# Optimization experiments

Hardware: AMD Instinct MI355X
Metric: run time of the kernel (lower is better)

The kernel has to match this reference:

```python
import jax, jax.numpy as jnp
import numpy as np
from jax import lax

B, DIM, H, W = 2, 128, 192, 192
GS = [16, 32, 32, 48]          # group ratios [1,2,2,3]/8 of DIM
HID = int(DIM * 2.66)          # 340, Restormer-style hidden width


def _pool_mat(n_in, n_out):
    # torch AdaptiveAvgPool as an explicit linear map [n_out, n_in]
    P = np.zeros((n_out, n_in), np.float32)
    for o in range(n_out):
        s = (o * n_in) // n_out
        e = ((o + 1) * n_in + n_out - 1) // n_out
        P[o, s:e] = 1.0 / (e - s)
    return jnp.asarray(P)


def _ln(t, w, b):
    # WithBias LayerNorm over the channel dim of NCHW (== LN over last dim of b(hw)c)
    mu = t.mean(1, keepdims=True)
    var = ((t - mu) ** 2).mean(1, keepdims=True)
    return (t - mu) / jnp.sqrt(var + 1e-5) * w[None, :, None, None] + b[None, :, None, None]


def _c1x1(t, w):
    return jnp.einsum('oc,bchw->bohw', w, t)


def _dw3(t, w):
    return lax.conv_general_dilated(t, w, (1, 1), 'SAME',
                                    dimension_numbers=('NCHW', 'OIHW', 'NCHW'),
                                    feature_group_count=t.shape[1])


def _c1d(t, w, b):
    return jnp.einsum('oc,bcl->bol', w, t) + b[None, :, None]


def _gelu(t):
    return jax.nn.gelu(t, approximate=False)


def _forward(x, qv_cache, ln1_w, ln1_b, ln2_w, ln2_b, temperature, w_qkv, w_qkv_dw, w_proj,
             intra_down_w, intra_down_b, intra_up_w, intra_up_b, intra_gate_w, intra_gate_b,
             inter0_cw_w, inter0_cw_b, inter0_g_w, inter0_g_b,
             inter1_cw_w, inter1_cw_b, inter1_g_w, inter1_g_b,
             inter2_cw_w, inter2_cw_b, inter2_g_w, inter2_g_b,
             inter3_cw_w, inter3_cw_b, inter3_g_w, inter3_g_b,
             ffn_in_w, ffn_dw_w, ffn_out_w):
    b, c, h, w_ = x.shape
    hw = h * w_
    inter_p = [(inter0_cw_w, inter0_cw_b, inter0_g_w, inter0_g_b),
               (inter1_cw_w, inter1_cw_b, inter1_g_w, inter1_g_b),
               (inter2_cw_w, inter2_cw_b, inter2_g_w, inter2_g_b),
               (inter3_cw_w, inter3_cw_b, inter3_g_w, inter3_g_b)]
    # ---- attention branch ----
    xn = _ln(x, ln1_w, ln1_b)
    qkv = _dw3(_c1x1(xn, w_qkv), w_qkv_dw)
    q, k, v = jnp.split(qkv, 3, axis=1)
    q = q.reshape(b, c, hw); k = k.reshape(b, c, hw); v = v.reshape(b, c, hw)
    # correlation-based channel re-grouping (torch.corrcoef on batch-mean of q)
    cf = q.mean(0)                                   # [C, HW]
    xm = cf - cf.mean(1, keepdims=True)
    cov = xm @ xm.T
    dsd = jnp.sqrt(jnp.diagonal(cov))
    corr = cov / (dsd[:, None] * dsd[None, :])
    idx = jnp.argsort(-corr.mean(1))                 # descending mean similarity
    q = q[:, idx]; k = k[:, idx]; v = v[:, idx]
    atts, tmpc, outs = [], [], []
    start = 0
    for i, g in enumerate(GS):
        qg = q[:, start:start + g]; kg = k[:, start:start + g]; vg = v[:, start:start + g]
        start += g
        qn = qg / jnp.maximum(jnp.linalg.norm(qg, axis=-1, keepdims=True), 1e-12)
        kn = kg / jnp.maximum(jnp.linalg.norm(kg, axis=-1, keepdims=True), 1e-12)
        att = jax.nn.softmax(jnp.einsum('bcl,bdl->bcd', qn, kn) * temperature[i, 0, 0], axis=-1)
        tmpc.append(lax.stop_gradient(qn) + lax.stop_gradient(kn))
        # Inter_CacheModulation: adaptive-pool cache to [g,g], FiLM + gated conv1d
        cw_w, cw_b, g_w, g_b = inter_p[i]
        P = _pool_mat(c, g)
        aligned = jnp.einsum('oi,bij,pj->bop', P, qv_cache, P)    # [1, g, g]
        scale, shift = jnp.split(_c1d(aligned + att, cw_w, cw_b), 2, axis=1)
        x1p = att * scale + shift
        att = x1p * _gelu(_c1d(x1p, g_w, g_b)) + att
        atts.append(att)
        outs.append(jnp.einsum('bcd,bdl->bcl', att, vg))
    # CalculateCurrentLayerCache: resize each group's batch-mean attn to [C,C].
    # Original does (u * c_i) // dim with c_i == dim, i.e. elementwise floor.
    acc = jnp.zeros((1, c, c), x.dtype)
    for a in atts:
        m = lax.stop_gradient(a).mean(0, keepdims=True)[:, None]  # [1,1,g,g]
        u = jax.image.resize(m, (1, 1, c, c), method='bilinear')
        acc = acc + jnp.floor(u)[:, 0]
    qv_new = qv_cache * 0.9 + acc * 0.1
    out_all = jnp.concatenate(outs, axis=1)          # [B, C, HW]
    tmp_all = jnp.concatenate(tmpc, axis=1)
    # Intra_CacheModulation
    s = tmp_all + out_all
    gated = _gelu(_c1d(s, intra_gate_w, intra_gate_b)) * s
    out_all = _c1d(_c1d(gated, intra_down_w, intra_down_b), intra_up_w, intra_up_b) + out_all
    x1 = x + _c1x1(out_all.reshape(b, c, h, w_), w_proj)
    # ---- gated-dconv FFN ----
    xn2 = _ln(x1, ln2_w, ln2_b)
    y1, y2 = jnp.split(_dw3(_c1x1(xn2, ffn_in_w), ffn_dw_w), 2, axis=1)
    out = x1 + _c1x1(_gelu(y1) * y2, ffn_out_w)
    return out, qv_new


def setup_inputs() -> dict:
    key = jax.random.key(0)
    ks = jax.random.split(key, 40)
    def w(i, shape, s=0.02):
        return jax.random.normal(ks[i], shape, jnp.float32) * s
    p = {}
    p['x'] = jax.random.normal(ks[0], (B, DIM, H, W), jnp.float32)
    p['qv_cache'] = jax.random.uniform(ks[1], (1, DIM, DIM), jnp.float32)
    p['ln1_w'] = jnp.ones((DIM,), jnp.float32); p['ln1_b'] = jnp.zeros((DIM,), jnp.float32)
    p['ln2_w'] = jnp.ones((DIM,), jnp.float32); p['ln2_b'] = jnp.zeros((DIM,), jnp.float32)
    p['temperature'] = jnp.ones((4, 1, 1), jnp.float32)
    p['w_qkv'] = w(2, (3 * DIM, DIM))
    p['w_qkv_dw'] = w(3, (3 * DIM, 1, 3, 3))
    p['w_proj'] = w(4, (DIM, DIM))
    p['intra_down_w'] = w(5, (DIM // 2, DIM)); p['intra_down_b'] = jnp.zeros((DIM // 2,), jnp.float32)
    p['intra_up_w'] = w(6, (DIM, DIM // 2)); p['intra_up_b'] = jnp.zeros((DIM,), jnp.float32)
    p['intra_gate_w'] = w(7, (DIM, DIM)); p['intra_gate_b'] = jnp.zeros((DIM,), jnp.float32)
    for i, g in enumerate(GS):
        p[f'inter{i}_cw_w'] = w(8 + 2 * i, (2 * g, g))
        p[f'inter{i}_cw_b'] = jnp.zeros((2 * g,), jnp.float32)
        p[f'inter{i}_g_w'] = w(9 + 2 * i, (g, g))
        p[f'inter{i}_g_b'] = jnp.zeros((g,), jnp.float32)
    p['ffn_in_w'] = w(20, (2 * HID, DIM))
    p['ffn_dw_w'] = w(21, (2 * HID, 1, 3, 3))
    p['ffn_out_w'] = w(22, (DIM, HID))
    return p


def reference(x, qv_cache, ln1_w, ln1_b, ln2_w, ln2_b, temperature, w_qkv, w_qkv_dw, w_proj,
              intra_down_w, intra_down_b, intra_up_w, intra_up_b, intra_gate_w, intra_gate_b,
              inter0_cw_w, inter0_cw_b, inter0_g_w, inter0_g_b,
              inter1_cw_w, inter1_cw_b, inter1_g_w, inter1_g_b,
              inter2_cw_w, inter2_cw_b, inter2_g_w, inter2_g_b,
              inter3_cw_w, inter3_cw_b, inter3_g_w, inter3_g_b,
              ffn_in_w, ffn_dw_w, ffn_out_w):
    return _forward(x, qv_cache, ln1_w, ln1_b, ln2_w, ln2_b, temperature, w_qkv, w_qkv_dw, w_proj,
                    intra_down_w, intra_down_b, intra_up_w, intra_up_b, intra_gate_w, intra_gate_b,
                    inter0_cw_w, inter0_cw_b, inter0_g_w, inter0_g_b,
                    inter1_cw_w, inter1_cw_b, inter1_g_w, inter1_g_b,
                    inter2_cw_w, inter2_cw_b, inter2_g_w, inter2_g_b,
                    inter3_cw_w, inter3_cw_b, inter3_g_w, inter3_g_b,
                    ffn_in_w, ffn_dw_w, ffn_out_w)
```

## Files before the change

### kernel.cpp

```cpp
#include <hip/hip_runtime.h>
#include <math.h>

#define TPB 256

constexpr int BN_  = 2;
constexpr int CDIM = 128;
constexpr int HH   = 192;
constexpr int WW   = 192;
constexpr int HWc  = HH * WW;
constexpr int C3   = 384;
constexpr int HID  = 340;
constexpr int NL2  = 288;
constexpr int CH2  = HWc / NL2;
constexpr int CV   = 288;

typedef unsigned short bf16_t;
typedef __attribute__((ext_vector_type(8))) __bf16 bf16x8;
typedef __attribute__((ext_vector_type(4))) float f32x4;

__device__ __forceinline__ float b2f(bf16_t v) {
  unsigned u = ((unsigned)v) << 16;
  return __uint_as_float(u);
}
__device__ __forceinline__ bf16_t f2b(float f) {
  unsigned u = __float_as_uint(f);
  unsigned r = (u + 0x7FFFu + ((u >> 16) & 1u)) >> 16;
  return (bf16_t)r;
}
__device__ __forceinline__ float ldf(const float* p) { return *p; }
__device__ __forceinline__ float ldf(const bf16_t* p) { return b2f(*p); }
__device__ __forceinline__ void stf(float* p, float v) { *p = v; }
__device__ __forceinline__ void stf(bf16_t* p, float v) { *p = f2b(v); }

__device__ __forceinline__ void ldv4(const float* p, float* v) {
  float4 t = *(const float4*)p;
  v[0] = t.x; v[1] = t.y; v[2] = t.z; v[3] = t.w;
}
__device__ __forceinline__ void ldv4(const bf16_t* p, float* v) {
  ushort4 t = *(const ushort4*)p;
  v[0] = b2f(t.x); v[1] = b2f(t.y); v[2] = b2f(t.z); v[3] = b2f(t.w);
}
__device__ __forceinline__ void stv4(float* p, const float* v) {
  float4 t; t.x = v[0]; t.y = v[1]; t.z = v[2]; t.w = v[3];
  *(float4*)p = t;
}
__device__ __forceinline__ void stv4(bf16_t* p, const float* v) {
  ushort4 t; t.x = f2b(v[0]); t.y = f2b(v[1]); t.z = f2b(v[2]); t.w = f2b(v[3]);
  *(ushort4*)p = t;
}

__device__ __forceinline__ float gelu_f(float x) {
  return 0.5f * x * (1.0f + erff(x * 0.7071067811865475f));
}

__device__ __forceinline__ void unpack8(uint4 v, float* rv) {
  unsigned wv[4] = {v.x, v.y, v.z, v.w};
#pragma unroll
  for (int j = 0; j < 8; ++j)
    rv[j + 1] = b2f((bf16_t)((wv[j >> 1] >> ((j & 1) * 16)) & 0xFFFFu));
}
__device__ __forceinline__ uint4 pack8(const float* a) {
  uint4 o;
  unsigned w[4];
#pragma unroll
  for (int p = 0; p < 4; ++p) {
    unsigned lo = f2b(a[2 * p]), hi = f2b(a[2 * p + 1]);
    w[p] = lo | (hi << 16);
  }
  o.x = w[0]; o.y = w[1]; o.z = w[2]; o.w = w[3];
  return o;
}
__device__ __forceinline__ float sum8(uint4 v) {
  unsigned w[4] = {v.x, v.y, v.z, v.w};
  float s = 0.f;
#pragma unroll
  for (int j = 0; j < 8; ++j)
    s += b2f((bf16_t)((w[j >> 1] >> ((j & 1) * 16)) & 0xFFFFu));
  return s;
}
__device__ __forceinline__ float sumsq8(uint4 v) {
  unsigned w[4] = {v.x, v.y, v.z, v.w};
  float s = 0.f;
#pragma unroll
  for (int j = 0; j < 8; ++j) {
    float t = b2f((bf16_t)((w[j >> 1] >> ((j & 1) * 16)) & 0xFFFFu));
    s += t * t;
  }
  return s;
}

__device__ __forceinline__ void dwrow(const bf16_t* rp, int w8, float* rv) {
  unpack8(*(const uint4*)rp, rv);
  rv[0] = (w8 > 0) ? b2f(rp[-1]) : 0.f;
  rv[9] = (w8 + 8 < WW) ? b2f(rp[8]) : 0.f;
}

__device__ __constant__ int dGSZ[4]   = {16, 32, 32, 48};
__device__ __constant__ int dGST[4]   = {0, 16, 48, 80};
__device__ __constant__ int dAOFF[4]  = {0, 256, 1280, 2304};
__device__ __constant__ int dABASE[4] = {0, 512, 2560, 4608};

constexpr size_t oATTRAW  = 0;
constexpr size_t oATTS2   = 65536;
constexpr size_t oMUP     = 102400;
constexpr size_t oWB      = 131072;
constexpr size_t oATTS    = 1327104;
constexpr size_t oNORMQ   = 1363968;
constexpr size_t oNORMK   = 1364992;
constexpr size_t oIDX     = 1366016;
constexpr size_t oMU      = 1366528;
constexpr size_t oCOV     = 1367040;
constexpr size_t oQKV     = 1572864;
constexpr size_t oXN      = 58195968;
constexpr size_t oOUTALL  = 77070336;
constexpr size_t oSBUF    = 95944704;
constexpr size_t WS_NEED  = 114819072;
constexpr size_t oCHUNK1  = oOUTALL;
constexpr size_t oCOVPART = oOUTALL;
constexpr size_t oCOVP2   = oSBUF;
constexpr size_t oQKPART  = oXN;
constexpr size_t oGATED   = oQKV;
constexpr size_t oDBUF    = oQKV + 18874368;
constexpr size_t oY0C     = oOUTALL;
constexpr size_t oZ       = oQKV;
constexpr size_t oX1B     = oXN;

constexpr int eWQ   = 0;
constexpr int eGATE = 49152;
constexpr int eDOWN = 65536;
constexpr int eUP   = 73728;
constexpr int ePROJ = 81920;
constexpr int eFFI  = 98304;
constexpr int eFFO  = 185344;
constexpr int eTOT  = 234496;

__global__ __launch_bounds__(TPB) void k_wcvt(const float* __restrict__ wq,
                                              const float* __restrict__ gate,
                                              const float* __restrict__ down,
                                              const float* __restrict__ up,
                                              const float* __restrict__ proj,
                                              const float* __restrict__ ffi,
                                              const float* __restrict__ ffo,
                                              bf16_t* __restrict__ wb) {
  int t = blockIdx.x * TPB + threadIdx.x;
  if (t >= eTOT) return;
  int u = t;
  if (u < 49152) { wb[eWQ + u] = f2b(wq[u]); return; }
  u -= 49152;
  if (u < 16384) { wb[eGATE + u] = f2b(gate[u]); return; }
  u -= 16384;
  if (u < 8192)  { wb[eDOWN + u] = f2b(down[u]); return; }
  u -= 8192;
  if (u < 8192)  { wb[eUP + u] = f2b(up[u]); return; }
  u -= 8192;
  if (u < 16384) { wb[ePROJ + u] = f2b(proj[u]); return; }
  u -= 16384;
  if (u < 87040) { wb[eFFI + u] = f2b(ffi[u]); return; }
  u -= 87040;
  {
    int o = u / 384, k = u - o * 384;
    wb[eFFO + u] = (k < HID) ? f2b(ffo[o * HID + k]) : (bf16_t)0;
  }
}

template <typename TI>
__global__ __launch_bounds__(TPB) void k_ln(const TI* __restrict__ x,
                                            const float* __restrict__ w,
                                            const float* __restrict__ bias,
                                            bf16_t* __restrict__ out) {
  int t = blockIdx.x * TPB + threadIdx.x;
  if (t >= BN_ * HWc) return;
  int b = t / HWc, l = t - b * HWc;
  const TI* xb = x + (size_t)b * CDIM * HWc + l;
  float s = 0.f, s2 = 0.f;
#pragma unroll 4
  for (int c = 0; c < CDIM; ++c) { float v = ldf(&xb[(size_t)c * HWc]); s += v; s2 += v * v; }
  float mu  = s * (1.f / CDIM);
  float var = s2 * (1.f / CDIM) - mu * mu;
  float inv = 1.f / sqrtf(var + 1e-5f);
  bf16_t* ob = out + (size_t)b * CDIM * HWc + l;
#pragma unroll 4
  for (int c = 0; c < CDIM; ++c)
    stf(&ob[(size_t)c * HWc], (ldf(&xb[(size_t)c * HWc]) - mu) * inv * w[c] + bias[c]);
}

template <typename TO, typename TA, int KT, int EPI>
__global__ __launch_bounds__(TPB) void k_mgA(const bf16_t* __restrict__ W,
                                             const bf16_t* __restrict__ W2, int osplit,
                                             const float* __restrict__ bias,
                                             const bf16_t* __restrict__ in,
                                             const TA* __restrict__ aux,
                                             TO* __restrict__ out, int O,
                                             int ibr, int obr, int abr) {
  constexpr int L  = HWc;
  constexpr int PK = KT + 8;
  constexpr int KH = KT / 2;
  constexpr int SH = (KT == 128) ? 6 : 5;
  __shared__ bf16_t At[128 * PK];
  __shared__ bf16_t Wt[64 * PK];
  int b = blockIdx.y;
  const bf16_t* inb  = in  + (size_t)b * ibr * L;
  const TA*     auxb = aux ? aux + (size_t)b * abr * L : nullptr;
  TO*           outb = out + (size_t)b * obr * L;
  int l0 = blockIdx.x * 128;
  int tid = threadIdx.x, lane = tid & 63, wid = tid >> 6;
  int wm = wid >> 1, wn = wid & 1;
  int cl = lane & 15, rg = lane >> 4;

#pragma unroll
  for (int r = 0; r < (KH * 16) / TPB; ++r) {
    int u  = tid + r * TPB;
    int k2 = u & (KH - 1), lb = u >> SH;
    int ka = k2 * 2;
    uint4 rowA = *(const uint4*)(&inb[(size_t)ka * L + l0 + lb * 8]);
    uint4 rowB = *(const uint4*)(&inb[(size_t)(ka + 1) * L + l0 + lb * 8]);
    unsigned wa[4] = {rowA.x, rowA.y, rowA.z, rowA.w};
    unsigned wb[4] = {rowB.x, rowB.y, rowB.z, rowB.w};
#pragma unroll
    for (int j = 0; j < 8; ++j) {
      unsigned va = (wa[j >> 1] >> ((j & 1) * 16)) & 0xFFFFu;
      unsigned vb = (wb[j >> 1] >> ((j & 1) * 16)) & 0xFFFFu;
      *(unsigned*)(&At[(lb * 8 + j) * PK + ka]) = va | (vb << 16);
    }
  }

  int noc = (O + 63) >> 6;
  for (int oc = 0; oc < noc; ++oc) {
    int o0 = oc * 64;
#pragma unroll
    for (int r = 0; r < (64 * KT / 8) / TPB; ++r) {
      int e = tid + r * TPB;
      int o = e / (KT / 8), k8 = (e % (KT / 8)) * 8;
      int og = o0 + o;
      uint4 wv = {0u, 0u, 0u, 0u};
      if (og < O) {
        const bf16_t* wrow = (og < osplit) ? (W + (size_t)og * KT)
                                           : (W2 + (size_t)(og - osplit) * KT);
        wv = *(const uint4*)(&wrow[k8]);
      }
      *(uint4*)(&Wt[o * PK + k8]) = wv;
    }
    __syncthreads();
    f32x4 acc[2][4];
#pragma unroll
    for (int m = 0; m < 2; ++m)
#pragma unroll
      for (int n = 0; n < 4; ++n) acc[m][n] = (f32x4){0.f, 0.f, 0.f, 0.f};
#pragma unroll
    for (int kk = 0; kk < KT / 32; ++kk) {
      int kof = kk * 32 + rg * 8;
      bf16x8 a[2], bfr[4];
#pragma unroll
      for (int m = 0; m < 2; ++m)
        a[m] = *(const bf16x8*)(&Wt[(wm * 32 + m * 16 + cl) * PK + kof]);
#pragma unroll
      for (int n = 0; n < 4; ++n)
        bfr[n] = *(const bf16x8*)(&At[(wn * 64 + n * 16 + cl) * PK + kof]);
#pragma unroll
// ... 25 lines not shown
          for (int r = 0; r < 4; ++r) v[r] = gelu_f(v[r]) * a4[r];
        } else if (EPI == 3) {
          int lloc = wn * 64 + n * 16 + rg * 4;
#pragma unroll
          for (int r = 0; r < 4; ++r)
            v[r] = gelu_f(v[r]) * b2f(At[(lloc + r) * PK + og]);
        }
        stv4(&outb[off], v);
      }
    }
  }
}

template <typename TO, typename TA, int EPI>
__global__ __launch_bounds__(TPB) void k_mgB(const bf16_t* __restrict__ Wb,
                                             const float* __restrict__ bias,
                                             const bf16_t* __restrict__ in,
                                             const TA* __restrict__ aux,
                                             TO* __restrict__ out, int O, int K,
                                             int ibr, int obr, int abr) {
  constexpr int L = HWc;
  constexpr int PK = 72, BK = 64, WSTR = 384;
  __shared__ bf16_t At[128 * PK];
  __shared__ bf16_t Wt[128 * PK];
  int b = blockIdx.y;
  const bf16_t* inb  = in  + (size_t)b * ibr * L;
  const TA*     auxb = aux ? aux + (size_t)b * abr * L : nullptr;
  TO*           outb = out + (size_t)b * obr * L;
  int l0 = blockIdx.x * 128;
  int tid = threadIdx.x, lane = tid & 63, wid = tid >> 6;
  int wm = wid >> 1, wn = wid & 1;
  int cl = lane & 15, rg = lane >> 4;

  f32x4 acc[4][4];
#pragma unroll
  for (int m = 0; m < 4; ++m)
#pragma unroll
    for (int n = 0; n < 4; ++n) acc[m][n] = (f32x4){0.f, 0.f, 0.f, 0.f};

  for (int k0 = 0; k0 < K; k0 += BK) {
#pragma unroll
    for (int r = 0; r < 2; ++r) {
      int u = tid + r * TPB;
      int k2 = u & 31, lb = u >> 5;
      int ka = k0 + k2 * 2;
      uint4 rowA = {0u,0u,0u,0u}, rowB = {0u,0u,0u,0u};
      if (ka < K)     rowA = *(const uint4*)(&inb[(size_t)ka * L + l0 + lb * 8]);
      if (ka + 1 < K) rowB = *(const uint4*)(&inb[(size_t)(ka + 1) * L + l0 + lb * 8]);
      unsigned wa[4] = {rowA.x, rowA.y, rowA.z, rowA.w};
      unsigned wb[4] = {rowB.x, rowB.y, rowB.z, rowB.w};
#pragma unroll
      for (int j = 0; j < 8; ++j) {
        unsigned va = (wa[j >> 1] >> ((j & 1) * 16)) & 0xFFFFu;
        unsigned vb = (wb[j >> 1] >> ((j & 1) * 16)) & 0xFFFFu;
        *(unsigned*)(&At[(lb * 8 + j) * PK + k2 * 2]) = va | (vb << 16);
      }
    }
#pragma unroll
    for (int r = 0; r < 4; ++r) {
      int e = tid + r * TPB;
      int o = e >> 3, k8 = (e & 7) * 8;
      uint4 wv = *(const uint4*)(&Wb[(size_t)o * WSTR + k0 + k8]);
      *(uint4*)(&Wt[o * PK + k8]) = wv;
    }
    __syncthreads();
#pragma unroll
    for (int kk = 0; kk < 2; ++kk) {
      int kof = kk * 32 + rg * 8;
      bf16x8 a[4], bfr[4];
#pragma unroll
      for (int m = 0; m < 4; ++m)
        a[m] = *(const bf16x8*)(&Wt[(wm * 64 + m * 16 + cl) * PK + kof]);
#pragma unroll
      for (int n = 0; n < 4; ++n)
        bfr[n] = *(const bf16x8*)(&At[(wn * 64 + n * 16 + cl) * PK + kof]);
#pragma unroll
      for (int m = 0; m < 4; ++m)
#pragma unroll
        for (int n = 0; n < 4; ++n)
          acc[m][n] = __builtin_amdgcn_mfma_f32_16x16x32_bf16(bfr[n], a[m], acc[m][n], 0, 0, 0);
    }
    __syncthreads();
  }
#pragma unroll
  for (int m = 0; m < 4; ++m) {
    int og = wm * 64 + m * 16 + cl;
    if (og >= O) continue;
    float bv = bias ? bias[og] : 0.f;
#pragma unroll
    for (int n = 0; n < 4; ++n) {
      int lcol = l0 + wn * 64 + n * 16 + rg * 4;
      size_t off = (size_t)og * L + lcol;
      float v[4];
#pragma unroll
      for (int r = 0; r < 4; ++r) v[r] = acc[m][n][r] + bv;
      if (EPI == 1) {
        float a4[4]; ldv4(&auxb[off], a4);
#pragma unroll
        for (int r = 0; r < 4; ++r) v[r] += a4[r];
      } else if (EPI == 2) {
        float a4[4]; ldv4(&auxb[off], a4);
#pragma unroll
        for (int r = 0; r < 4; ++r) v[r] = gelu_f(v[r]) * a4[r];
      }
      stv4(&outb[off], v);
    }
  }
}

__global__ __launch_bounds__(TPB) void k_dw3v(const bf16_t* __restrict__ in,
                                              const float* __restrict__ wt,
                                              bf16_t* __restrict__ out,
                                              int Cc, int c0, int CoutTotal, long totalG) {
  long t = (long)blockIdx.x * TPB + threadIdx.x;
  if (t >= totalG) return;
  int g = (int)(t % (HWc / 16));
  long bc = t / (HWc / 16);
  int cl = (int)(bc % Cc);
  int b = (int)(bc / Cc);
  int rp = g / (WW / 8), w8 = (g % (WW / 8)) * 8;
  int h = rp * 2;
  const bf16_t* ib = in + ((size_t)b * Cc + cl) * HWc;
  const float* wc = wt + (size_t)(c0 + cl) * 9;
  float rv[4][10];
#pragma unroll
  for (int dy = 0; dy < 4; ++dy) {
    int hh = h - 1 + dy;
    if (hh < 0 || hh >= HH) {
#pragma unroll
      for (int j = 0; j < 10; ++j) rv[dy][j] = 0.f;
    } else {
      dwrow(ib + hh * WW + w8, w8, rv[dy]);
    }
  }
  float a0[8], a1[8];
#pragma unroll
  for (int j = 0; j < 8; ++j) {
    float s0 = 0.f, s1 = 0.f;
#pragma unroll
    for (int dy = 0; dy < 3; ++dy)
#pragma unroll
      for (int dx = 0; dx < 3; ++dx) {
        float wv = wc[dy * 3 + dx];
        s0 += rv[dy][j + dx] * wv;
        s1 += rv[dy + 1][j + dx] * wv;
      }
    a0[j] = s0; a1[j] = s1;
  }
  bf16_t* ob = out + ((size_t)b * CoutTotal + c0 + cl) * HWc + h * WW + w8;
  *(uint4*)ob = pack8(a0);
  *(uint4*)(ob + WW) = pack8(a1);
}

__global__ __launch_bounds__(TPB) void k_mu1(const bf16_t* __restrict__ qkv,
                                             float* __restrict__ mupart) {
  int c = blockIdx.x, ch = blockIdx.y;
  int tid = threadIdx.x;
  int base = ch * (HWc / 8);
  __shared__ float red[TPB];
  float s = 0.f;
  for (int u = tid; u < (HWc / 8) / 8; u += TPB) {
    uint4 v0 = *(const uint4*)(&qkv[(size_t)c * HWc + base + u * 8]);
    uint4 v1 = *(const uint4*)(&qkv[(size_t)C3 * HWc + (size_t)c * HWc + base + u * 8]);
    s += 0.5f * (sum8(v0) + sum8(v1));
  }
  red[tid] = s;
  __syncthreads();
  for (int st = TPB / 2; st > 0; st >>= 1) {
    if (tid < st) red[tid] += red[tid + st];
    __syncthreads();
  }
  if (tid == 0) mupart[c * 8 + ch] = red[0];
}
__global__ __launch_bounds__(CDIM) void k_mured(const float* __restrict__ mupart,
                                                float* __restrict__ mu) {
  int c = threadIdx.x;
  float s = 0.f;
#pragma unroll
  for (int ch = 0; ch < 8; ++ch) s += mupart[c * 8 + ch];
  mu[c] = s / HWc;
}

__global__ __launch_bounds__(TPB) void k_cov4(const bf16_t* __restrict__ qkv,
                                              float* __restrict__ part) {
  constexpr int PK = 136;
  __shared__ bf16_t Xt[128 * PK];
  int chunk = blockIdx.x;
  int base = chunk * 128;
  int tid = threadIdx.x, lane = tid & 63, wid = tid >> 6;
  int wm = wid >> 1, wn = wid & 1;
  int cl = lane & 15, rg = lane >> 4;
#pragma unroll
  for (int r = 0; r < 8; ++r) {
    int u = tid + r * TPB;
    int c = u >> 4, l8 = (u & 15) * 8;
    uint4 v0 = *(const uint4*)(&qkv[(size_t)c * HWc + base + l8]);
    uint4 v1 = *(const uint4*)(&qkv[(size_t)C3 * HWc + (size_t)c * HWc + base + l8]);
    unsigned w0[4] = {v0.x, v0.y, v0.z, v0.w};
    unsigned w1[4] = {v1.x, v1.y, v1.z, v1.w};
    float cf[8];
#pragma unroll
    for (int j = 0; j < 8; ++j) {
      float a = b2f((bf16_t)((w0[j >> 1] >> ((j & 1) * 16)) & 0xFFFFu));
      float bq = b2f((bf16_t)((w1[j >> 1] >> ((j & 1) * 16)) & 0xFFFFu));
      cf[j] = 0.5f * (a + bq);
    }
    *(uint4*)(&Xt[c * PK + l8]) = pack8(cf);
  }
  __syncthreads();
  f32x4 acc[4][4];
#pragma unroll
  for (int m = 0; m < 4; ++m)
#pragma unroll
    for (int n = 0; n < 4; ++n) acc[m][n] = (f32x4){0.f, 0.f, 0.f, 0.f};
#pragma unroll
  for (int kk = 0; kk < 4; ++kk) {
    int kof = kk * 32 + rg * 8;
    bf16x8 a[4], bfr[4];
#pragma unroll
    for (int m = 0; m < 4; ++m)
      a[m] = *(const bf16x8*)(&Xt[(wm * 64 + m * 16 + cl) * PK + kof]);
#pragma unroll
    for (int n = 0; n < 4; ++n)
      bfr[n] = *(const bf16x8*)(&Xt[(wn * 64 + n * 16 + cl) * PK + kof]);
#pragma unroll
    for (int m = 0; m < 4; ++m)
#pragma unroll
      for (int n = 0; n < 4; ++n)
        acc[m][n] = __builtin_amdgcn_mfma_f32_16x16x32_bf16(bfr[n], a[m], acc[m][n], 0, 0, 0);
  }
  float* pb = part + (size_t)chunk * CDIM * CDIM;
#pragma unroll
  for (int m = 0; m < 4; ++m) {
    int c = wm * 64 + m * 16 + cl;
#pragma unroll
    for (int n = 0; n < 4; ++n) {
      int d0 = wn * 64 + n * 16 + rg * 4;
      float v[4] = {acc[m][n][0], acc[m][n][1], acc[m][n][2], acc[m][n][3]};
      stv4(&pb[c * CDIM + d0], v);
    }
  }
}

__global__ __launch_bounds__(TPB) void k_covred1(const float* __restrict__ part,
                                                 float* __restrict__ p2) {
  int t = blockIdx.x * TPB + threadIdx.x;
  int yg = blockIdx.y;
  float s = 0.f;
  for (int p = yg * 36; p < (yg + 1) * 36; ++p)
    s += part[(size_t)p * CDIM * CDIM + t];
  p2[(size_t)yg * CDIM * CDIM + t] = s;
}
__global__ __launch_bounds__(TPB) void k_covred2(const float* __restrict__ p2,
                                                 const float* __restrict__ mu,
                                                 float* __restrict__ cov) {
  int t = blockIdx.x * TPB + threadIdx.x;
  if (t >= CDIM * CDIM) return;
  float s = 0.f;
#pragma unroll
  for (int y = 0; y < 8; ++y) s += p2[(size_t)y * CDIM * CDIM + t];
  int c = t >> 7, d = t & 127;
  cov[t] = s - (float)HWc * mu[c] * mu[d];
}

__global__ __launch_bounds__(CDIM) void k_rank(const float* __restrict__ cov,
                                               int* __restrict__ idx) {
  __shared__ float dsd[CDIM], score[CDIM];
  int tid = threadIdx.x;
  dsd[tid] = sqrtf(cov[tid * CDIM + tid]);
  __syncthreads();
  {
    float s = 0.f, di = dsd[tid];
    for (int d = 0; d < CDIM; ++d) s += cov[tid * CDIM + d] / (di * dsd[d]);
    score[tid] = s;
  }
  __syncthreads();
  {
    float my = score[tid];
    int rank = 0;
    for (int d = 0; d < CDIM; ++d)
      rank += (score[d] > my) || (score[d] == my && d < tid);
    idx[rank] = tid;
  }
}

__global__ __launch_bounds__(TPB) void k_norms(const bf16_t* __restrict__ qkv,
                                               const int* __restrict__ idx,
                                               float* __restrict__ invq,
                                               float* __restrict__ invk) {
  int p = blockIdx.x, b = blockIdx.y, which = blockIdx.z;
  int ch = idx[p] + which * CDIM;
  const bf16_t* row = qkv + ((size_t)b * C3 + ch) * HWc;
  __shared__ float red[TPB];
  float s = 0.f;
  for (int u = threadIdx.x; u < HWc / 8; u += TPB)
    s += sumsq8(*(const uint4*)(&row[u * 8]));
  red[threadIdx.x] = s;
  __syncthreads();
  for (int st = TPB / 2; st > 0; st >>= 1) {
    if (threadIdx.x < st) red[threadIdx.x] += red[threadIdx.x + st];
    __syncthreads();
  }
  if (threadIdx.x == 0) {
    float n = fmaxf(sqrtf(red[0]), 1e-12f);
    (which ? invk : invq)[b * CDIM + p] = 1.f / n;
  }
}

template <int G>
__device__ __forceinline__ void qk2_impl(char* sm, const bf16_t* __restrict__ qkv,
                                         const int* __restrict__ idx, int start,
                                         float* __restrict__ partial, int nl, int b) {
  constexpr int RT = G / 16;
  constexpr int U  = G * CH2 / 8;
  float (*qs)[CH2 + 2] = (float (*)[CH2 + 2])sm;
  float (*ks)[CH2 + 2] = (float (*)[CH2 + 2])(sm + (size_t)G * (CH2 + 2) * 4);
  int* idxg = (int*)(sm + (size_t)2 * G * (CH2 + 2) * 4);
  int tid = threadIdx.x;
  if (tid < G) idxg[tid] = idx[start + tid];
  __syncthreads();
  int l0 = nl * CH2;
  for (int u = tid; u < U; u += TPB) {
    int r = u / (CH2 / 8), c8 = (u % (CH2 / 8)) * 8;
    int ch = idxg[r];
    uint4 vq = *(const uint4*)(&qkv[((size_t)b * C3 + ch) * HWc + l0 + c8]);
    uint4 vk = *(const uint4*)(&qkv[((size_t)b * C3 + CDIM + ch) * HWc + l0 + c8]);
    unsigned wq[4] = {vq.x, vq.y, vq.z, vq.w};
    unsigned wk[4] = {vk.x, vk.y, vk.z, vk.w};
#pragma unroll
    for (int j = 0; j < 8; ++j) {
      qs[r][c8 + j] = b2f((bf16_t)((wq[j >> 1] >> ((j & 1) * 16)) & 0xFFFFu));
      ks[r][c8 + j] = b2f((bf16_t)((wk[j >> 1] >> ((j & 1) * 16)) & 0xFFFFu));
    }
  }
  __syncthreads();
  int ti = tid & 15, tj = tid >> 4;
  float acc[RT][RT];
#pragma unroll
  for (int m = 0; m < RT; ++m)
#pragma unroll
    for (int n = 0; n < RT; ++n) acc[m][n] = 0.f;
#pragma unroll 4
  for (int l = 0; l < CH2; ++l) {
    float qa[RT], kb[RT];
#pragma unroll
    for (int m = 0; m < RT; ++m) qa[m] = qs[ti * RT + m][l];
#pragma unroll
    for (int n = 0; n < RT; ++n) kb[n] = ks[tj * RT + n][l];
#pragma unroll
    for (int m = 0; m < RT; ++m)
#pragma unroll
      for (int n = 0; n < RT; ++n) acc[m][n] += qa[m] * kb[n];
  }
  float* pb = partial + ((size_t)(b * NL2) + nl) * G * G;
#pragma unroll
  for (int m = 0; m < RT; ++m)
#pragma unroll
    for (int n = 0; n < RT; ++n)
      pb[(ti * RT + m) * G + tj * RT + n] = acc[m][n];
}

__global__ __launch_bounds__(TPB) void k_qk2g(const bf16_t* __restrict__ qkv,
                                              const int* __restrict__ idx,
                                              float* __restrict__ qkpart) {
  extern __shared__ char sm[];
  int nl = blockIdx.x, b = blockIdx.y, gi = blockIdx.z;
  if (gi == 0)      qk2_impl<16>(sm, qkv, idx, 0,  qkpart + 0,       nl, b);
  else if (gi == 1) qk2_impl<32>(sm, qkv, idx, 16, qkpart + 147456,  nl, b);
  else if (gi == 2) qk2_impl<32>(sm, qkv, idx, 48, qkpart + 737280,  nl, b);
  else              qk2_impl<48>(sm, qkv, idx, 80, qkpart + 1327104, nl, b);
}

__global__ __launch_bounds__(TPB) void k_qkredg(const float* __restrict__ qkpart,
                                                float* __restrict__ attraw) {
  int t = blockIdx.x * TPB + threadIdx.x;
  if (t >= BN_ * 4608) return;
  int b = t / 4608, e = t - b * 4608;
  int gi = (e < 256) ? 0 : (e < 1280) ? 1 : (e < 2304) ? 2 : 3;
  const int gg4[4]    = {256, 1024, 1024, 2304};
  const int pgoff[4]  = {0, 147456, 737280, 1327104};
  const int aoff4[4]  = {0, 256, 1280, 2304};
  int GGg = gg4[gi];
  int el = e - aoff4[gi];
  const float* pb = qkpart + pgoff[gi] + (size_t)(b * NL2) * GGg + el;
  float s = 0.f;
  for (int nl = 0; nl < NL2; ++nl) s += pb[(size_t)nl * GGg];
  attraw[t] = s;
}

__global__ __launch_bounds__(TPB) void k_smg(const float* __restrict__ attraw,
                                             const float* __restrict__ invq,
                                             const float* __restrict__ invk,
                                             const float* __restrict__ temperature,
                                             float* __restrict__ attS) {
  int b = blockIdx.x, gi = blockIdx.y;
  int G = dGSZ[gi], start = dGST[gi];
  int GG = G * G;
  const float* ar = attraw + b * 4608 + dAOFF[gi];
  float* as = attS + b * 4608 + dAOFF[gi];
  float temp = temperature[gi];
  __shared__ float att[2304];
  int tid = threadIdx.x;
  for (int e = tid; e < GG; e += TPB) {
    int i = e / G, j = e - i * G;
    att[e] = ar[e] * temp * invq[b * CDIM + start + i] * invk[b * CDIM + start + j];
  }
  __syncthreads();
  if (tid < G) {
    float mx = -3.4e38f;
    for (int j = 0; j < G; ++j) mx = fmaxf(mx, att[tid * G + j]);
    float ssum = 0.f;
    for (int j = 0; j < G; ++j) { float ex = expf(att[tid * G + j] - mx); att[tid * G + j] = ex; ssum += ex; }
    float inv = 1.f / ssum;
    for (int j = 0; j < G; ++j) att[tid * G + j] *= inv;
  }
  __syncthreads();
  for (int e = tid; e < GG; e += TPB) as[e] = att[e];
}

__global__ __launch_bounds__(TPB) void k_imlpg(const float* __restrict__ attS,
                                               const float* __restrict__ qv_cache,
                                               const float* __restrict__ cw0, const float* __restrict__ cb0,
                                               const float* __restrict__ gw0, const float* __restrict__ gb0,
                                               const float* __restrict__ cw1, const float* __restrict__ cb1,
                                               const float* __restrict__ gw1, const float* __restrict__ gb1,
                                               const float* __restrict__ cw2, const float* __restrict__ cb2,
                                               const float* __restrict__ gw2, const float* __restrict__ gb2,
                                               const float* __restrict__ cw3, const float* __restrict__ cb3,
                                               const float* __restrict__ gw3, const float* __restrict__ gb3,
                                               float* __restrict__ attF) {
  int b = blockIdx.x, gi = blockIdx.y, tile = blockIdx.z;
  int G = dGSZ[gi];
  int p0 = tile * 16;
  if (p0 >= G) return;
  int GG = G * G;
  const float* cw_w = (gi == 0) ? cw0 : (gi == 1) ? cw1 : (gi == 2) ? cw2 : cw3;
  const float* cw_b = (gi == 0) ? cb0 : (gi == 1) ? cb1 : (gi == 2) ? cb2 : cb3;
  const float* g_w  = (gi == 0) ? gw0 : (gi == 1) ? gw1 : (gi == 2) ? gw2 : gw3;
  const float* g_b  = (gi == 0) ? gb0 : (gi == 1) ? gb1 : (gi == 2) ? gb2 : gb3;
  const float* as = attS + b * 4608 + dAOFF[gi];
  float* af = attF + dABASE[gi] + (size_t)b * GG;
  int tid = threadIdx.x;
  __shared__ float cwW[2 * 48 * 48];
  __shared__ float gW[48 * 48];
  __shared__ float attC[48 * 16], t1C[48 * 16], scC[48 * 16], shC[48 * 16],
                   x1pC[48 * 16], t2C[48 * 16];
  for (int e = tid; e < 2 * G * G; e += TPB) cwW[e] = cw_w[e];
  for (int e = tid; e < G * G; e += TPB) gW[e] = g_w[e];
  for (int u = tid; u < G * 16; u += TPB) {
    int c = u >> 4, pl = u & 15;
    int p = p0 + pl;
    float av = 0.f, pv = 0.f;
    if (p < G) {
      av = as[c * G + p];
      int so = c * CDIM / G, eo = ((c + 1) * CDIM + G - 1) / G;
      int sp = p * CDIM / G, ep = ((p + 1) * CDIM + G - 1) / G;
      float ssum = 0.f;
      for (int i2 = so; i2 < eo; ++i2)
        for (int j2 = sp; j2 < ep; ++j2) ssum += qv_cache[i2 * CDIM + j2];
      pv = ssum / (float)((eo - so) * (ep - sp));
    }
    attC[u] = av;
    t1C[u] = pv + av;
  }
  __syncthreads();
  for (int u = tid; u < 2 * G * 16; u += TPB) {
    int o = u >> 4, pl = u & 15;
    float acc = cw_b[o];
    for (int c = 0; c < G; ++c) acc += cwW[o * G + c] * t1C[c * 16 + pl];
    if (o < G) scC[o * 16 + pl] = acc;
    else       shC[(o - G) * 16 + pl] = acc;
  }
  __syncthreads();
  for (int u = tid; u < G * 16; u += TPB)
    x1pC[u] = attC[u] * scC[u] + shC[u];
  __syncthreads();
  for (int u = tid; u < G * 16; u += TPB) {
    int o = u >> 4, pl = u & 15;
    float acc = g_b[o];
    for (int c = 0; c < G; ++c) acc += gW[o * G + c] * x1pC[c * 16 + pl];
    t2C[u] = acc;
  }
  __syncthreads();
  for (int u = tid; u < G * 16; u += TPB) {
    int c = u >> 4, pl = u & 15;
    int p = p0 + pl;
    if (p < G)
      af[c * G + p] = x1pC[u] * gelu_f(t2C[u]) + attC[u];
  }
}

template <int G, int GP>
__device__ __forceinline__ void av2_impl(char* sm, const bf16_t* __restrict__ qkv,
                                         const int* __restrict__ idx,
                                         const float* __restrict__ attF,
                                         const float* __restrict__ invq,
                                         const float* __restrict__ invk, int start,
                                         bf16_t* __restrict__ out_all,
                                         bf16_t* __restrict__ s_buf, int l0, int b) {
  constexpr int PK = GP + 8;
  constexpr int MT = G / 16;
  bf16_t* Vt = (bf16_t*)sm;
  bf16_t* Ab = (bf16_t*)(sm + (size_t)128 * PK * 2);
  int* idxg  = (int*)(sm + (size_t)128 * PK * 2 + (size_t)G * PK * 2);
  int tid = threadIdx.x, lane = tid & 63, wid = tid >> 6;
  int cl = lane & 15, rg = lane >> 4;
  if (tid < G) idxg[tid] = idx[start + tid];
  __syncthreads();
  for (int u = tid; u < (GP / 2) * 16; u += TPB) {
    int j2 = u % (GP / 2), lb = u / (GP / 2);
    int ja = j2 * 2;
    uint4 rA = {0u,0u,0u,0u}, rB = {0u,0u,0u,0u};
    if (ja < G)     rA = *(const uint4*)(&qkv[((size_t)b * C3 + 2 * CDIM + idxg[ja]) * HWc + l0 + lb * 8]);
    if (ja + 1 < G) rB = *(const uint4*)(&qkv[((size_t)b * C3 + 2 * CDIM + idxg[ja + 1]) * HWc + l0 + lb * 8]);
    unsigned wa[4] = {rA.x, rA.y, rA.z, rA.w};
    unsigned wb[4] = {rB.x, rB.y, rB.z, rB.w};
#pragma unroll
    for (int j = 0; j < 8; ++j) {
      unsigned va = (wa[j >> 1] >> ((j & 1) * 16)) & 0xFFFFu;
      unsigned vb = (wb[j >> 1] >> ((j & 1) * 16)) & 0xFFFFu;
      *(unsigned*)(&Vt[(lb * 8 + j) * PK + ja]) = va | (vb << 16);
    }
  }
  for (int e = tid; e < G * GP; e += TPB) {
    int p = e / GP, j = e - p * GP;
    Ab[p * PK + j] = (j < G) ? f2b(attF[(size_t)b * G * G + p * G + j]) : (bf16_t)0;
  }
  __syncthreads();
  f32x4 acc[MT][2];
#pragma unroll
  for (int m = 0; m < MT; ++m)
#pragma unroll
    for (int n = 0; n < 2; ++n) acc[m][n] = (f32x4){0.f, 0.f, 0.f, 0.f};
#pragma unroll
  for (int kk = 0; kk < GP / 32; ++kk) {
    int kof = kk * 32 + rg * 8;
    bf16x8 a[MT], bfr[2];
#pragma unroll
    for (int m = 0; m < MT; ++m)
      a[m] = *(const bf16x8*)(&Ab[(m * 16 + cl) * PK + kof]);
#pragma unroll
    for (int n = 0; n < 2; ++n)
      bfr[n] = *(const bf16x8*)(&Vt[(wid * 32 + n * 16 + cl) * PK + kof]);
#pragma unroll
    for (int m = 0; m < MT; ++m)
#pragma unroll
      for (int n = 0; n < 2; ++n)
        acc[m][n] = __builtin_amdgcn_mfma_f32_16x16x32_bf16(bfr[n], a[m], acc[m][n], 0, 0, 0);
  }
#pragma unroll
  for (int m = 0; m < MT; ++m) {
    int p = m * 16 + cl;
    int pg = start + p;
    int ch = idxg[p];
    float iq = invq[b * CDIM + pg], ik = invk[b * CDIM + pg];
#pragma unroll
    for (int n = 0; n < 2; ++n) {
      int lg = l0 + wid * 32 + n * 16 + rg * 4;
      float q4[4], k4[4];
      ldv4(&qkv[((size_t)b * C3 + ch) * HWc + lg], q4);
      ldv4(&qkv[((size_t)b * C3 + CDIM + ch) * HWc + lg], k4);
      float vo[4], vs[4];
#pragma unroll
      for (int r = 0; r < 4; ++r) {
        vo[r] = acc[m][n][r];
        vs[r] = vo[r] + q4[r] * iq + k4[r] * ik;
      }
      size_t off = ((size_t)b * CDIM + pg) * HWc + lg;
      stv4(&out_all[off], vo);
      stv4(&s_buf[off], vs);
    }
  }
}

__global__ __launch_bounds__(TPB) void k_avg(const bf16_t* __restrict__ qkv,
                                             const int* __restrict__ idx,
                                             const float* __restrict__ atts,
                                             const float* __restrict__ invq,
                                             const float* __restrict__ invk,
                                             bf16_t* __restrict__ out_all,
                                             bf16_t* __restrict__ s_buf) {
  extern __shared__ char sm[];
  int l0 = blockIdx.x * 128, b = blockIdx.y, gi = blockIdx.z;
  if (gi == 0)      av2_impl<16, 32>(sm, qkv, idx, atts + 0,    invq, invk, 0,  out_all, s_buf, l0, b);
  else if (gi == 1) av2_impl<32, 32>(sm, qkv, idx, atts + 512,  invq, invk, 16, out_all, s_buf, l0, b);
  else if (gi == 2) av2_impl<32, 32>(sm, qkv, idx, atts + 2560, invq, invk, 48, out_all, s_buf, l0, b);
  else              av2_impl<48, 64>(sm, qkv, idx, atts + 4608, invq, invk, 80, out_all, s_buf, l0, b);
}

__global__ __launch_bounds__(TPB) void k_qvnew(const float* __restrict__ attsF,
                                               const float* __restrict__ qv_cache,
                                               float* __restrict__ out_qv) {
  int t = blockIdx.x * TPB + threadIdx.x;
  if (t >= CDIM * CDIM) return;
  int r = t >> 7, cq = t & 127;
  const int gs[4]   = {16, 32, 32, 48};
  const int base[4] = {0, 512, 2560, 4608};
  float acc = 0.f;
  for (int gi = 0; gi < 4; ++gi) {
    int g = gs[gi], gg = g * g;
    const float* a0 = attsF + base[gi];
    float scale = (float)g / CDIM;
    float fr = (r + 0.5f) * scale - 0.5f;
    float fc = (cq + 0.5f) * scale - 0.5f;
    float flr = floorf(fr), flc = floorf(fc);
    int i0 = (int)flr, j0 = (int)flc;
    float wr = fr - flr, wcw = fc - flc;
    int i0c = max(i0, 0), i1c = min(i0 + 1, g - 1);
    int j0c = max(j0, 0), j1c = min(j0 + 1, g - 1);
    float m00 = 0.5f * (a0[i0c * g + j0c] + a0[gg + i0c * g + j0c]);
    float m01 = 0.5f * (a0[i0c * g + j1c] + a0[gg + i0c * g + j1c]);
    float m10 = 0.5f * (a0[i1c * g + j0c] + a0[gg + i1c * g + j0c]);
    float m11 = 0.5f * (a0[i1c * g + j1c] + a0[gg + i1c * g + j1c]);
    float val = (1.f - wr) * ((1.f - wcw) * m00 + wcw * m01)
              + wr * ((1.f - wcw) * m10 + wcw * m11);
    acc += floorf(val);
  }
  out_qv[t] = qv_cache[t] * 0.9f + acc * 0.1f;
}

__global__ __launch_bounds__(TPB) void k_dwgeluv(const bf16_t* __restrict__ y0c,
                                                 const float* __restrict__ wt,
                                                 bf16_t* __restrict__ z,
                                                 int Cc, int c0, long totalG) {
  long t = (long)blockIdx.x * TPB + threadIdx.x;
  if (t >= totalG) return;
  int g = (int)(t % (HWc / 16));
  long bc = t / (HWc / 16);
  int cl = (int)(bc % Cc);
  int b = (int)(bc / Cc);
  int rp = g / (WW / 8), w8 = (g % (WW / 8)) * 8;
  int h = rp * 2;
  const bf16_t* i1 = y0c + ((size_t)b * 2 * Cc + cl) * HWc;
  const bf16_t* i2 = i1 + (size_t)Cc * HWc;
  const float* w1 = wt + (size_t)(c0 + cl) * 9;
  const float* w2 = wt + (size_t)(HID + c0 + cl) * 9;
  float rv[4][10];
#pragma unroll
  for (int dy = 0; dy < 4; ++dy) {
    int hh = h - 1 + dy;
    if (hh < 0 || hh >= HH) {
#pragma unroll
      for (int j = 0; j < 10; ++j) rv[dy][j] = 0.f;
    } else {
      dwrow(i1 + hh * WW + w8, w8, rv[dy]);
    }
  }
  float g0[8], g1[8];
#pragma unroll
  for (int j = 0; j < 8; ++j) {
    float s0 = 0.f, s1 = 0.f;
#pragma unroll
    for (int dy = 0; dy < 3; ++dy)
#pragma unroll
      for (int dx = 0; dx < 3; ++dx) {
        float wv = w1[dy * 3 + dx];
        s0 += rv[dy][j + dx] * wv;
        s1 += rv[dy + 1][j + dx] * wv;
      }
    g0[j] = gelu_f(s0); g1[j] = gelu_f(s1);
  }
#pragma unroll
  for (int dy = 0; dy < 4; ++dy) {
    int hh = h - 1 + dy;
    if (hh < 0 || hh >= HH) {
#pragma unroll
      for (int j = 0; j < 10; ++j) rv[dy][j] = 0.f;
    } else {
      dwrow(i2 + hh * WW + w8, w8, rv[dy]);
    }
  }
  float o0[8], o1[8];
#pragma unroll
  for (int j = 0; j < 8; ++j) {
    float s0 = 0.f, s1 = 0.f;
#pragma unroll
    for (int dy = 0; dy < 3; ++dy)
#pragma unroll
      for (int dx = 0; dx < 3; ++dx) {
        float wv = w2[dy * 3 + dx];
        s0 += rv[dy][j + dx] * wv;
        s1 += rv[dy + 1][j + dx] * wv;
      }
    o0[j] = g0[j] * s0; o1[j] = g1[j] * s1;
  }
  bf16_t* zp = z + ((size_t)b * HID + c0 + cl) * HWc + h * WW + w8;
  *(uint4*)zp = pack8(o0);
  *(uint4*)(zp + WW) = pack8(o1);
}

extern "C" void kernel_launch(void* const* d_in, const int* in_sizes, int n_in,
                              void* d_out, int out_size, void* d_ws, size_t ws_size,
                              hipStream_t stream) {
  if (ws_size < WS_NEED) return;

  const float* x        = (const float*)d_in[0];
  const float* qv_cache = (const float*)d_in[1];
  const float* ln1_w    = (const float*)d_in[2];
  const float* ln1_b    = (const float*)d_in[3];
  const float* ln2_w    = (const float*)d_in[4];
  const float* ln2_b    = (const float*)d_in[5];
  const float* temperature = (const float*)d_in[6];
  const float* w_qkv    = (const float*)d_in[7];
  const float* w_qkv_dw = (const float*)d_in[8];
  const float* w_proj   = (const float*)d_in[9];
  const float* intra_down_w = (const float*)d_in[10];
  const float* intra_down_b = (const float*)d_in[11];
  const float* intra_up_w   = (const float*)d_in[12];
  const float* intra_up_b   = (const float*)d_in[13];
  const float* intra_gate_w = (const float*)d_in[14];
  const float* intra_gate_b = (const float*)d_in[15];
  const float* ffn_in_w  = (const float*)d_in[32];
  const float* ffn_dw_w  = (const float*)d_in[33];
  const float* ffn_out_w = (const float*)d_in[34];

  char* wsb = (char*)d_ws;
  float* out    = (float*)d_out;
  float* out_qv = out + (size_t)BN_ * CDIM * HWc;
  bf16_t* xn2   = (bf16_t*)d_out;

  float*  attraw  = (float*)(wsb + oATTRAW);
  float*  attS    = (float*)(wsb + oATTS2);
  float*  mupart  = (float*)(wsb + oMUP);
  bf16_t* wb      = (bf16_t*)(wsb + oWB);
  float*  atts    = (float*)(wsb + oATTS);
  float*  invqA   = (float*)(wsb + oNORMQ);
  float*  invkA   = (float*)(wsb + oNORMK);
  int*    idx     = (int*)(wsb + oIDX);
  float*  mu      = (float*)(wsb + oMU);
  float*  cov     = (float*)(wsb + oCOV);
  bf16_t* qkv     = (bf16_t*)(wsb + oQKV);
  bf16_t* xn      = (bf16_t*)(wsb + oXN);
  bf16_t* out_all = (bf16_t*)(wsb + oOUTALL);
  bf16_t* sbuf    = (bf16_t*)(wsb + oSBUF);
  bf16_t* chunk1  = (bf16_t*)(wsb + oCHUNK1);
  float*  covpart = (float*)(wsb + oCOVPART);
  float*  covp2   = (float*)(wsb + oCOVP2);
  float*  qkpart  = (float*)(wsb + oQKPART);
  bf16_t* gated   = (bf16_t*)(wsb + oGATED);
  bf16_t* dbuf    = (bf16_t*)(wsb + oDBUF);
  bf16_t* x1b     = (bf16_t*)(wsb + oX1B);
  bf16_t* y0c     = (bf16_t*)(wsb + oY0C);
  bf16_t* zbuf    = (bf16_t*)(wsb + oZ);

  const bf16_t* wq_b   = wb + eWQ;
  const bf16_t* gate_b = wb + eGATE;
  const bf16_t* down_b = wb + eDOWN;
  const bf16_t* up_b   = wb + eUP;
  const bf16_t* proj_b = wb + ePROJ;
  const bf16_t* ffi_b  = wb + eFFI;
  const bf16_t* ffo_b  = wb + eFFO;

  const int GX = HWc / 128;
  const int NOS = 1 << 30;
  dim3 gA(GX, BN_);

  k_wcvt<<<(eTOT + TPB - 1) / TPB, TPB, 0, stream>>>(
      w_qkv, intra_gate_w, intra_down_w, intra_up_w, w_proj, ffn_in_w, ffn_out_w, wb);

  k_ln<float><<<(BN_ * HWc + TPB - 1) / TPB, TPB, 0, stream>>>(x, ln1_w, ln1_b, xn);

  for (int ci = 0; ci < 2; ++ci) {
    int c0 = ci * 192;
    k_mgA<bf16_t, float, 128, 0><<<gA, TPB, 0, stream>>>(
        wq_b + (size_t)c0 * CDIM, wq_b, NOS, nullptr, xn, nullptr, chunk1,
        192, CDIM, 192, 0);
    long totG = (long)BN_ * 192 * (HWc / 16);
    k_dw3v<<<(unsigned)((totG + TPB - 1) / TPB), TPB, 0, stream>>>(
        chunk1, w_qkv_dw, qkv, 192, c0, C3, totG);
  }

  k_mu1<<<dim3(CDIM, 8), TPB, 0, stream>>>(qkv, mupart);
  k_mured<<<1, CDIM, 0, stream>>>(mupart, mu);
  k_cov4<<<CV, TPB, 0, stream>>>(qkv, covpart);
  k_covred1<<<dim3(64, 8), TPB, 0, stream>>>(covpart, covp2);
  k_covred2<<<64, TPB, 0, stream>>>(covp2, mu, cov);
  k_rank<<<1, CDIM, 0, stream>>>(cov, idx);
  k_norms<<<dim3(CDIM, BN_, 2), TPB, 0, stream>>>(qkv, idx, invqA, invkA);

  {
    size_t dyn = (size_t)2 * 48 * (CH2 + 2) * 4 + 48 * 4;
    k_qk2g<<<dim3(NL2, BN_, 4), TPB, dyn, stream>>>(qkv, idx, qkpart);
  }
  k_qkredg<<<(BN_ * 4608 + TPB - 1) / TPB, TPB, 0, stream>>>(qkpart, attraw);
  k_smg<<<dim3(BN_, 4), TPB, 0, stream>>>(attraw, invqA, invkA, temperature, attS);
  k_imlpg<<<dim3(BN_, 4, 3), TPB, 0, stream>>>(
      attS, qv_cache,
      (const float*)d_in[16], (const float*)d_in[17], (const float*)d_in[18], (const float*)d_in[19],
      (const float*)d_in[20], (const float*)d_in[21], (const float*)d_in[22], (const float*)d_in[23],
      (const float*)d_in[24], (const float*)d_in[25], (const float*)d_in[26], (const float*)d_in[27],
      (const float*)d_in[28], (const float*)d_in[29], (const float*)d_in[30], (const float*)d_in[31],
      atts);
  {
    size_t dyn = (size_t)128 * 72 * 2 + (size_t)48 * 72 * 2 + 48 * 4;
    k_avg<<<dim3(HWc / 128, BN_, 4), TPB, dyn, stream>>>(
        qkv, idx, atts, invqA, invkA, out_all, sbuf);
  }
  k_qvnew<<<(CDIM * CDIM + TPB - 1) / TPB, TPB, 0, stream>>>(atts, qv_cache, out_qv);

  k_mgA<bf16_t, float, 128, 3><<<gA, TPB, 0, stream>>>(
      gate_b, gate_b, NOS, intra_gate_b, sbuf, nullptr, gated,
      CDIM, CDIM, CDIM, 0);
  k_mgA<bf16_t, float, 128, 0><<<gA, TPB, 0, stream>>>(
      down_b, down_b, NOS, intra_down_b, gated, nullptr, dbuf,
      CDIM / 2, CDIM, CDIM / 2, 0);
  k_mgA<bf16_t, bf16_t, 64, 1><<<gA, TPB, 0, stream>>>(
      up_b, up_b, NOS, intra_up_b, dbuf, out_all, out_all,
      CDIM, CDIM / 2, CDIM, CDIM);
  k_mgA<bf16_t, float, 128, 1><<<gA, TPB, 0, stream>>>(
      proj_b, proj_b, NOS, nullptr, out_all, x, x1b, CDIM, CDIM, CDIM, CDIM);
  k_ln<bf16_t><<<(BN_ * HWc + TPB - 1) / TPB, TPB, 0, stream>>>(x1b, ln2_w, ln2_b, xn2);

  const int fcc[3] = {114, 114, 112};
  const int fc0[3] = {0, 114, 228};
  for (int ci = 0; ci < 3; ++ci) {
    int Cc = fcc[ci], c0 = fc0[ci];
    k_mgA<bf16_t, float, 128, 0><<<gA, TPB, 0, stream>>>(
        ffi_b + (size_t)c0 * CDIM, ffi_b + (size_t)(HID + c0) * CDIM, Cc,
        nullptr, xn2, nullptr, y0c, 2 * Cc, CDIM, 2 * Cc, 0);
    long totG = (long)BN_ * Cc * (HWc / 16);
    k_dwgeluv<<<(unsigned)((totG + TPB - 1) / TPB), TPB, 0, stream>>>(
        y0c, ffn_dw_w, zbuf, Cc, c0, totG);
  }
  k_mgB<float, bf16_t, 1><<<gA, TPB, 0, stream>>>(
      ffo_b, nullptr, zbuf, x1b, out, CDIM, HID, HID, CDIM, CDIM);
}
```

Baseline: 516.4 us.

## Fuse channel-mean into covariance kernel, decouple norms from rank, split qk reduction

```diff
diff --git a/kernel.cpp b/kernel.cpp
--- a/kernel.cpp
+++ b/kernel.cpp
@@ -70,14 +70,6 @@
   o.x = w[0]; o.y = w[1]; o.z = w[2]; o.w = w[3];
   return o;
 }
-__device__ __forceinline__ float sum8(uint4 v) {
-  unsigned w[4] = {v.x, v.y, v.z, v.w};
-  float s = 0.f;
-#pragma unroll
-  for (int j = 0; j < 8; ++j)
-    s += b2f((bf16_t)((w[j >> 1] >> ((j & 1) * 16)) & 0xFFFFu));
-  return s;
-}
 __device__ __forceinline__ float sumsq8(uint4 v) {
   unsigned w[4] = {v.x, v.y, v.z, v.w};
   float s = 0.f;
@@ -102,8 +94,9 @@
 
 constexpr size_t oATTRAW  = 0;
 constexpr size_t oATTS2   = 65536;
-constexpr size_t oMUP     = 102400;
 constexpr size_t oWB      = 131072;
+constexpr size_t oQKP2    = 602112;
+constexpr size_t oMUPC    = 897024;
 constexpr size_t oATTS    = 1327104;
 constexpr size_t oNORMQ   = 1363968;
 constexpr size_t oNORMK   = 1364992;
@@ -435,37 +428,9 @@
   *(uint4*)(ob + WW) = pack8(a1);
 }
 
-__global__ __launch_bounds__(TPB) void k_mu1(const bf16_t* __restrict__ qkv,
-                                             float* __restrict__ mupart) {
-  int c = blockIdx.x, ch = blockIdx.y;
-  int tid = threadIdx.x;
-  int base = ch * (HWc / 8);
-  __shared__ float red[TPB];
-  float s = 0.f;
-  for (int u = tid; u < (HWc / 8) / 8; u += TPB) {
-    uint4 v0 = *(const uint4*)(&qkv[(size_t)c * HWc + base + u * 8]);
-    uint4 v1 = *(const uint4*)(&qkv[(size_t)C3 * HWc + (size_t)c * HWc + base + u * 8]);
-    s += 0.5f * (sum8(v0) + sum8(v1));
-  }
-  red[tid] = s;
-  __syncthreads();
-  for (int st = TPB / 2; st > 0; st >>= 1) {
-    if (tid < st) red[tid] += red[tid + st];
-    __syncthreads();
-  }
-  if (tid == 0) mupart[c * 8 + ch] = red[0];
-}
-__global__ __launch_bounds__(CDIM) void k_mured(const float* __restrict__ mupart,
-                                                float* __restrict__ mu) {
-  int c = threadIdx.x;
-  float s = 0.f;
-#pragma unroll
-  for (int ch = 0; ch < 8; ++ch) s += mupart[c * 8 + ch];
-  mu[c] = s / HWc;
-}
-
 __global__ __launch_bounds__(TPB) void k_cov4(const bf16_t* __restrict__ qkv,
-                                              float* __restrict__ part) {
+                                              float* __restrict__ part,
+                                              float* __restrict__ mupartC) {
   constexpr int PK = 136;
   __shared__ bf16_t Xt[128 * PK];
   int chunk = blockIdx.x;
@@ -491,6 +456,14 @@
     *(uint4*)(&Xt[c * PK + l8]) = pack8(cf);
   }
   __syncthreads();
+  {
+    int c = tid >> 1, half = tid & 1;
+    float s = 0.f;
+    for (int l = half * 64; l < half * 64 + 64; ++l)
+      s += b2f(Xt[c * PK + l]);
+    s += __shfl_xor(s, 1, 64);
+    if (half == 0) mupartC[(size_t)chunk * CDIM + c] = s;
+  }
   f32x4 acc[4][4];
 #pragma unroll
   for (int m = 0; m < 4; ++m)
@@ -523,6 +496,22 @@
       stv4(&pb[c * CDIM + d0], v);
     }
   }
+}
+
+__global__ __launch_bounds__(TPB) void k_muredC(const float* __restrict__ mupartC,
+                                                float* __restrict__ mu) {
+  int c = blockIdx.x;
+  int tid = threadIdx.x;
+  __shared__ float red[TPB];
+  float s = 0.f;
+  for (int u = tid; u < CV; u += TPB) s += mupartC[(size_t)u * CDIM + c];
+  red[tid] = s;
+  __syncthreads();
+  for (int st = TPB / 2; st > 0; st >>= 1) {
+    if (tid < st) red[tid] += red[tid + st];
+    __syncthreads();
+  }
+  if (tid == 0) mu[c] = red[0] / HWc;
 }
 
 __global__ __launch_bounds__(TPB) void k_covred1(const float* __restrict__ part,
@@ -568,12 +557,10 @@
 }
 
 __global__ __launch_bounds__(TPB) void k_norms(const bf16_t* __restrict__ qkv,
-                                               const int* __restrict__ idx,
                                                float* __restrict__ invq,
                                                float* __restrict__ invk) {
-  int p = blockIdx.x, b = blockIdx.y, which = blockIdx.z;
-  int ch = idx[p] + which * CDIM;
-  const bf16_t* row = qkv + ((size_t)b * C3 + ch) * HWc;
+  int ch = blockIdx.x, b = blockIdx.y, which = blockIdx.z;
+  const bf16_t* row = qkv + ((size_t)b * C3 + which * CDIM + ch) * HWc;
   __shared__ float red[TPB];
   float s = 0.f;
   for (int u = threadIdx.x; u < HWc / 8; u += TPB)
@@ -586,7 +573,7 @@
   }
   if (threadIdx.x == 0) {
     float n = fmaxf(sqrtf(red[0]), 1e-12f);
-    (which ? invk : invq)[b * CDIM + p] = 1.f / n;
+    (which ? invk : invq)[b * CDIM + ch] = 1.f / n;
   }
 }
 
@@ -654,10 +641,10 @@
   else              qk2_impl<48>(sm, qkv, idx, 80, qkpart + 1327104, nl, b);
 }
 
-__global__ __launch_bounds__(TPB) void k_qkredg(const float* __restrict__ qkpart,
-                                                float* __restrict__ attraw) {
+__global__ __launch_bounds__(TPB) void k_qkred1(const float* __restrict__ qkpart,
+                                                float* __restrict__ qkp2) {
   int t = blockIdx.x * TPB + threadIdx.x;
-  if (t >= BN_ * 4608) return;
+  int yg = blockIdx.y;
   int b = t / 4608, e = t - b * 4608;
   int gi = (e < 256) ? 0 : (e < 1280) ? 1 : (e < 2304) ? 2 : 3;
   const int gg4[4]    = {256, 1024, 1024, 2304};
@@ -667,11 +654,21 @@
   int el = e - aoff4[gi];
   const float* pb = qkpart + pgoff[gi] + (size_t)(b * NL2) * GGg + el;
   float s = 0.f;
-  for (int nl = 0; nl < NL2; ++nl) s += pb[(size_t)nl * GGg];
+  for (int nl = yg * 36; nl < (yg + 1) * 36; ++nl) s += pb[(size_t)nl * GGg];
+  qkp2[(size_t)yg * (BN_ * 4608) + t] = s;
+}
+__global__ __launch_bounds__(TPB) void k_qkred2(const float* __restrict__ qkp2,
+                                                float* __restrict__ attraw) {
+  int t = blockIdx.x * TPB + threadIdx.x;
+  if (t >= BN_ * 4608) return;
+  float s = 0.f;
+#pragma unroll
+  for (int y = 0; y < 8; ++y) s += qkp2[(size_t)y * (BN_ * 4608) + t];
   attraw[t] = s;
 }
 
 __global__ __launch_bounds__(TPB) void k_smg(const float* __restrict__ attraw,
+                                             const int* __restrict__ idx,
                                              const float* __restrict__ invq,
                                              const float* __restrict__ invk,
                                              const float* __restrict__ temperature,
@@ -683,10 +680,17 @@
   float* as = attS + b * 4608 + dAOFF[gi];
   float temp = temperature[gi];
   __shared__ float att[2304];
+  __shared__ float ivq[48], ivk[48];
   int tid = threadIdx.x;
+  if (tid < G) {
+    int ch = idx[start + tid];
+    ivq[tid] = invq[b * CDIM + ch];
+    ivk[tid] = invk[b * CDIM + ch];
+  }
+  __syncthreads();
   for (int e = tid; e < GG; e += TPB) {
     int i = e / G, j = e - i * G;
-    att[e] = ar[e] * temp * invq[b * CDIM + start + i] * invk[b * CDIM + start + j];
+    att[e] = ar[e] * temp * ivq[i] * ivk[j];
   }
   __syncthreads();
   if (tid < G) {
@@ -836,7 +840,7 @@
     int p = m * 16 + cl;
     int pg = start + p;
     int ch = idxg[p];
-    float iq = invq[b * CDIM + pg], ik = invk[b * CDIM + pg];
+    float iq = invq[b * CDIM + ch], ik = invk[b * CDIM + ch];
 #pragma unroll
     for (int n = 0; n < 2; ++n) {
       int lg = l0 + wid * 32 + n * 16 + rg * 4;
@@ -1004,8 +1008,9 @@
 
   float*  attraw  = (float*)(wsb + oATTRAW);
   float*  attS    = (float*)(wsb + oATTS2);
-  float*  mupart  = (float*)(wsb + oMUP);
   bf16_t* wb      = (bf16_t*)(wsb + oWB);
+  float*  qkp2    = (float*)(wsb + oQKP2);
+  float*  mupartC = (float*)(wsb + oMUPC);
   float*  atts    = (float*)(wsb + oATTS);
   float*  invqA   = (float*)(wsb + oNORMQ);
   float*  invkA   = (float*)(wsb + oNORMK);
@@ -1053,20 +1058,21 @@
         chunk1, w_qkv_dw, qkv, 192, c0, C3, totG);
   }
 
-  k_mu1<<<dim3(CDIM, 8), TPB, 0, stream>>>(qkv, mupart);
-  k_mured<<<1, CDIM, 0, stream>>>(mupart, mu);
-  k_cov4<<<CV, TPB, 0, stream>>>(qkv, covpart);
+  k_norms<<<dim3(CDIM, BN_, 2), TPB, 0, stream>>>(qkv, invqA, invkA);
+
+  k_cov4<<<CV, TPB, 0, stream>>>(qkv, covpart, mupartC);
+  k_muredC<<<CDIM, TPB, 0, stream>>>(mupartC, mu);
   k_covred1<<<dim3(64, 8), TPB, 0, stream>>>(covpart, covp2);
   k_covred2<<<64, TPB, 0, stream>>>(covp2, mu, cov);
   k_rank<<<1, CDIM, 0, stream>>>(cov, idx);
-  k_norms<<<dim3(CDIM, BN_, 2), TPB, 0, stream>>>(qkv, idx, invqA, invkA);
 
   {
     size_t dyn = (size_t)2 * 48 * (CH2 + 2) * 4 + 48 * 4;
     k_qk2g<<<dim3(NL2, BN_, 4), TPB, dyn, stream>>>(qkv, idx, qkpart);
   }
-  k_qkredg<<<(BN_ * 4608 + TPB - 1) / TPB, TPB, 0, stream>>>(qkpart, attraw);
-  k_smg<<<dim3(BN_, 4), TPB, 0, stream>>>(attraw, invqA, invkA, temperature, attS);
+  k_qkred1<<<dim3(36, 8), TPB, 0, stream>>>(qkpart, qkp2);
+  k_qkred2<<<36, TPB, 0, stream>>>(qkp2, attraw);
+  k_smg<<<dim3(BN_, 4), TPB, 0, stream>>>(attraw, idx, invqA, invkA, temperature, attS);
   k_imlpg<<<dim3(BN_, 4, 3), TPB, 0, stream>>>(
       attS, qv_cache,
       (const float*)d_in[16], (const float*)d_in[17], (const float*)d_in[18], (const float*)d_in[19],
```

Result: no change. 513.5 us (-0.6%).
